# Optimization experiments

Measured on AMD Instinct MI355X. Metric: run time of the kernel, lower is better.

## Reference

```python
import jax, jax.numpy as jnp
import numpy as np

B, S, D, H = 4, 1024, 1024, 16
HS = D // H  # head_size = 64


def setup_inputs() -> dict:
    key = jax.random.key(0)
    ks = jax.random.split(key, 6)
    scale = 1.0 / np.sqrt(D)
    data = jax.random.normal(ks[0], (B, S, D), dtype=jnp.float32)
    # Per-head projection weights, stacked: [H, D, HS] (no bias, per nn.Linear(bias=False))
    Wq = jax.random.normal(ks[1], (H, D, HS), dtype=jnp.float32) * scale
    Wk = jax.random.normal(ks[2], (H, D, HS), dtype=jnp.float32) * scale
    Wv = jax.random.normal(ks[3], (H, D, HS), dtype=jnp.float32) * scale
    # Output projection: [H*HS, D] plus bias [D]
    Wo = jax.random.normal(ks[4], (H * HS, D), dtype=jnp.float32) * scale
    bo = jax.random.normal(ks[5], (D,), dtype=jnp.float32) * 0.01
    return {"data": data, "Wq": Wq, "Wk": Wk, "Wv": Wv, "Wo": Wo, "bo": bo}


def reference(data, Wq, Wk, Wv, Wo, bo):
    b, s, d = data.shape
    # Per-head Q/K/V projections (self-attention: encoder_data = data)
    q = jnp.einsum('bsd,hde->bhse', data, Wq)  # [B,H,S,HS]
    k = jnp.einsum('bsd,hde->bhse', data, Wk)
    v = jnp.einsum('bsd,hde->bhse', data, Wv)
    # NOTE: original scales by sqrt(embedding_dimension), not sqrt(head_size)
    scores = jnp.einsum('bhse,bhte->bhst', q, k) / jnp.sqrt(jnp.asarray(d, dtype=data.dtype))
    # causal mask (tril of block_size, sliced to [S, S])
    causal = jnp.tril(jnp.ones((s, s), dtype=bool))
    scores = jnp.where(causal, scores, -jnp.inf)
    attn = jax.nn.softmax(scores, axis=-1)  # dropout rate 0.0 -> identity
    out = jnp.einsum('bhst,bhte->bhse', attn, v)  # [B,H,S,HS]
    # concat heads along feature dim (head order matches ModuleList order)
    out = out.transpose(0, 2, 1, 3).reshape(b, s, -1)  # [B,S,H*HS]
    return out @ Wo + bo
```

## Files before the change

### kernel.cpp

```cpp
#include <hip/hip_runtime.h>
#include <hip/hip_bf16.h>
#include <stdint.h>

#define NEG_SENTINEL (-1e30f)

typedef short s16x8 __attribute__((ext_vector_type(8)));
typedef float f32x4 __attribute__((ext_vector_type(4)));

__device__ __forceinline__ ushort f2bf(float f) {
  union { float f; uint32_t u; } v; v.f = f;
  uint32_t u = v.u;
  u += 0x7fffu + ((u >> 16) & 1u);
  return (ushort)(u >> 16);
}
__device__ __forceinline__ ushort f2bf_rn(float f) {
  union { float f; uint32_t u; } v; v.f = f;
  return (ushort)((v.u + 0x8000u) >> 16);
}

__device__ __forceinline__ void async_ld16(ushort* lds, const ushort* g) {
  __builtin_amdgcn_global_load_lds(
      (const __attribute__((address_space(1))) uint32_t*)g,
      (__attribute__((address_space(3))) uint32_t*)lds, 16, 0, 0);
}

__global__ __launch_bounds__(256) void convert_f32_bf16(
    const float* __restrict__ src, ushort* __restrict__ dst) {
  long i = ((long)blockIdx.x * 256 + threadIdx.x) * 8;
  float4 a = *(const float4*)(src + i);
  float4 b = *(const float4*)(src + i + 4);
  union { ushort u[8]; uint4 v; } o;
  o.u[0] = f2bf(a.x); o.u[1] = f2bf(a.y); o.u[2] = f2bf(a.z); o.u[3] = f2bf(a.w);
  o.u[4] = f2bf(b.x); o.u[5] = f2bf(b.y); o.u[6] = f2bf(b.z); o.u[7] = f2bf(b.w);
  *(uint4*)(dst + i) = o.v;
}

__global__ __launch_bounds__(256) void transpose_w3(
    const float* __restrict__ Wq, const float* __restrict__ Wk,
    const float* __restrict__ Wv, ushort* __restrict__ WTall) {
  const int z = blockIdx.z;
  const int matsel = z >> 4;
  const float* src = (matsel == 0 ? Wq : (matsel == 1 ? Wk : Wv)) +
                     (long)(z & 15) * 65536;
  ushort* dst = WTall + (long)z * 65536;
  const int it = blockIdx.y;
  __shared__ __align__(16) ushort tile[64 * 72];
  const int tid = threadIdx.x;
#pragma unroll
  for (int p = 0; p < 4; ++p) {
    int chunk = tid + p * 256;
    int r = chunk >> 4, c0 = (chunk & 15) * 4;
    float4 f = *(const float4*)(src + (long)(it * 64 + r) * 64 + c0);
    union { ushort u[4]; uint2 v; } o;
    o.u[0] = f2bf(f.x); o.u[1] = f2bf(f.y); o.u[2] = f2bf(f.z); o.u[3] = f2bf(f.w);
    *(uint2*)&tile[r * 72 + c0] = o.v;
  }
  __syncthreads();
#pragma unroll
  for (int p = 0; p < 2; ++p) {
    int chunk = tid + p * 256;
    int r = chunk >> 3, c0 = (chunk & 7) * 8;
    union { ushort u[8]; uint4 v; } tmp;
#pragma unroll
    for (int k2 = 0; k2 < 8; ++k2) tmp.u[k2] = tile[(c0 + k2) * 72 + r];
    *(uint4*)(dst + (long)r * 1024 + it * 64 + c0) = tmp.v;
  }
}

__global__ __launch_bounds__(256) void transpose_cvt(
    const float* __restrict__ src, ushort* __restrict__ dst) {
  const int jt = blockIdx.x;
  const int it = blockIdx.y;
  __shared__ __align__(16) ushort tile[64 * 72];
  const int tid = threadIdx.x;
#pragma unroll
  for (int p = 0; p < 4; ++p) {
    int chunk = tid + p * 256;
    int r = chunk >> 4, c0 = (chunk & 15) * 4;
    float4 f = *(const float4*)(src + (long)(it * 64 + r) * 1024 + jt * 64 + c0);
    union { ushort u[4]; uint2 v; } o;
    o.u[0] = f2bf(f.x); o.u[1] = f2bf(f.y); o.u[2] = f2bf(f.z); o.u[3] = f2bf(f.w);
    *(uint2*)&tile[r * 72 + c0] = o.v;
  }
  __syncthreads();
#pragma unroll
  for (int p = 0; p < 2; ++p) {
    int chunk = tid + p * 256;
    int r = chunk >> 3, c0 = (chunk & 7) * 8;
    union { ushort u[8]; uint4 v; } tmp;
#pragma unroll
    for (int k2 = 0; k2 < 8; ++k2) tmp.u[k2] = tile[(c0 + k2) * 72 + r];
    *(uint4*)(dst + (long)(jt * 64 + r) * 1024 + it * 64 + c0) = tmp.v;
  }
}

__device__ __forceinline__ void gemm_core_128x128(
    const ushort* __restrict__ A, const ushort* __restrict__ BT,
    ushort* As, ushort* Bs, f32x4 acc[4][4]) {
  const int tid = threadIdx.x;
  const int lane = tid & 63, w = tid >> 6, quad = lane >> 4, l15 = lane & 15;
  const int wm = w >> 1, wn = w & 1;
  for (int k0 = 0; k0 < 1024; k0 += 64) {
#pragma unroll
    for (int p = 0; p < 4; ++p) {
      int c = tid + p * 256;
      int r = c >> 3, c8 = (c & 7) * 8;
      async_ld16(As + c * 8, A + (long)r * 1024 + k0 + c8);
      async_ld16(Bs + c * 8, BT + (long)r * 1024 + k0 + c8);
    }
    __syncthreads();
#pragma unroll
    for (int kk = 0; kk < 64; kk += 32) {
      s16x8 af[4], bfr[4];
#pragma unroll
      for (int mi = 0; mi < 4; ++mi)
        af[mi] = *(const s16x8*)&As[(wm * 64 + mi * 16 + l15) * 64 + kk + quad * 8];
#pragma unroll
      for (int ni = 0; ni < 4; ++ni)
        bfr[ni] = *(const s16x8*)&Bs[(wn * 64 + ni * 16 + l15) * 64 + kk + quad * 8];
#pragma unroll
      for (int mi = 0; mi < 4; ++mi)
#pragma unroll
        for (int ni = 0; ni < 4; ++ni)
          acc[mi][ni] = __builtin_amdgcn_mfma_f32_16x16x32_bf16(
              af[mi], bfr[ni], acc[mi][ni], 0, 0, 0);
    }
    __syncthreads();
  }
}

__global__ __launch_bounds__(256) void qkv_proj(
    const ushort* __restrict__ dataB, const ushort* __restrict__ WTall,
    ushort* __restrict__ QKV) {
  __shared__ __align__(16) ushort smem[128 * 136];
  ushort* As = smem;
  ushort* Bs = smem + 8192;
  ushort* Ct = smem;
  const int m0 = blockIdx.x * 128;
  const int n0 = blockIdx.y * 128;
  f32x4 acc[4][4];
  const f32x4 z = {0.f, 0.f, 0.f, 0.f};
#pragma unroll
  for (int mi = 0; mi < 4; ++mi)
#pragma unroll
    for (int ni = 0; ni < 4; ++ni) acc[mi][ni] = z;
  gemm_core_128x128(dataB + (long)m0 * 1024, WTall + (long)n0 * 1024, As, Bs, acc);

  const int tid = threadIdx.x;
  const int lane = tid & 63, w = tid >> 6, quad = lane >> 4, l15 = lane & 15;
  const int wm = w >> 1, wn = w & 1;
  const int matsel = n0 >> 10;
  const int bI = m0 >> 10, s0 = m0 & 1023;

  if (matsel < 2) {
    const float sc = (matsel == 0) ? 0.03125f : 1.0f;
    ushort* base = QKV + (long)matsel * 4194304 + (long)bI * 1048576;
#pragma unroll
    for (int mi = 0; mi < 4; ++mi) {
#pragma unroll
      for (int ni = 0; ni < 4; ++ni) {
        int n = n0 + wn * 64 + ni * 16 + l15;
        int h = (n >> 6) & 15, e = n & 63;
        ushort* col = base + (long)h * 65536 + e;
#pragma unroll
        for (int i = 0; i < 4; ++i) {
          int s = s0 + wm * 64 + mi * 16 + quad * 4 + i;
          col[s * 64] = f2bf(acc[mi][ni][i] * sc);
        }
      }
    }
  } else {
#pragma unroll
    for (int mi = 0; mi < 4; ++mi)
#pragma unroll
      for (int ni = 0; ni < 4; ++ni)
#pragma unroll
        for (int i = 0; i < 4; ++i)
          Ct[(wn * 64 + ni * 16 + l15) * 136 + wm * 64 + mi * 16 + quad * 4 + i] =
              f2bf(acc[mi][ni][i]);
    __syncthreads();
    ushort* base = QKV + 8388608 + (long)bI * 1048576;
#pragma unroll
    for (int p = 0; p < 8; ++p) {
      int c = tid + p * 256;
      int r = c >> 4, m8 = (c & 15) * 8;
      int h = ((n0 + r) >> 6) & 15, e = (n0 + r) & 63;
      *(uint4*)(base + (long)h * 65536 + e * 1024 + s0 + m8) =
          *(const uint4*)&Ct[r * 136 + m8];
    }
  }
}

__global__ __launch_bounds__(256) void out_proj(
    const ushort* __restrict__ Ocat, const ushort* __restrict__ WoT,
    const float* __restrict__ bo, float* __restrict__ out) {
  __shared__ __align__(16) ushort As[128 * 64];
  __shared__ __align__(16) ushort Bs[128 * 64];
  const int m0 = blockIdx.x * 128;
  const int n0 = blockIdx.y * 128;
  f32x4 acc[4][4];
  const f32x4 z = {0.f, 0.f, 0.f, 0.f};
#pragma unroll
  for (int mi = 0; mi < 4; ++mi)
#pragma unroll
    for (int ni = 0; ni < 4; ++ni) acc[mi][ni] = z;
  gemm_core_128x128(Ocat + (long)m0 * 1024, WoT + (long)n0 * 1024, As, Bs, acc);

  const int tid = threadIdx.x;
  const int lane = tid & 63, w = tid >> 6, quad = lane >> 4, l15 = lane & 15;
  const int wm = w >> 1, wn = w & 1;
#pragma unroll
  for (int mi = 0; mi < 4; ++mi) {
#pragma unroll
    for (int ni = 0; ni < 4; ++ni) {
#pragma unroll
      for (int i = 0; i < 4; ++i) {
        int m = m0 + wm * 64 + mi * 16 + quad * 4 + i;
        int n = n0 + wn * 64 + ni * 16 + l15;
        out[(long)m * 1024 + n] = acc[mi][ni][i] + bo[n];
      }
    }
  }
}

__global__ __launch_bounds__(512, 4) void attn_kernel(
    const ushort* __restrict__ QKV, ushort* __restrict__ Ocat) {
  __shared__ __align__(16) ushort Ks[128 * 72];
  __shared__ __align__(16) ushort Vs[64 * 136];
  __shared__ __align__(16) ushort Ps[8 * 16 * 136];
  const int qt = 7 - blockIdx.y;
  const int bh = blockIdx.x;
  const int b = bh >> 4, h = bh & 15;
  const int tid = threadIdx.x;
  const int w = tid >> 6, lane = tid & 63, quad = lane >> 4, l15 = lane & 15;
  const int q0 = qt * 128;

  const ushort* Qp = QKV + (long)bh * 65536;
  const ushort* Kp = QKV + 4194304 + (long)bh * 65536;
  const ushort* VTp = QKV + 8388608 + (long)bh * 65536;

  const int qrow = q0 + w * 16 + l15;
  s16x8 qf0 = *(const s16x8*)(Qp + (long)qrow * 64 + quad * 8);
  s16x8 qf1 = *(const s16x8*)(Qp + (long)qrow * 64 + 32 + quad * 8);

  f32x4 oacc[4];
  const f32x4 z = {0.f, 0.f, 0.f, 0.f};
#pragma unroll
  for (int et = 0; et < 4; ++et) oacc[et] = z;
  float l_i[4] = {0.f, 0.f, 0.f, 0.f};

  ushort* Psw = Ps + w * (16 * 136);
  const int nj = qt + 1;

  for (int j = 0; j < nj; ++j) {
#pragma unroll
    for (int p = 0; p < 2; ++p) {
      int c = tid + p * 512;
      { int r = c >> 3, c8 = (c & 7) * 8;
        *(uint4*)&Ks[r * 72 + c8] = *(const uint4*)(Kp + (long)(j * 128 + r) * 64 + c8); }
      { int r = c >> 4, c8 = (c & 15) * 8;
        *(uint4*)&Vs[r * 136 + c8] = *(const uint4*)(VTp + (long)r * 1024 + j * 128 + c8); }
    }
    __syncthreads();

    f32x4 sacc[8];
#pragma unroll
    for (int nt = 0; nt < 8; ++nt) sacc[nt] = z;
#pragma unroll
    for (int kk = 0; kk < 64; kk += 32) {
      s16x8 a = kk ? qf1 : qf0;
#pragma unroll
      for (int nt = 0; nt < 8; ++nt) {
        s16x8 bfr = *(const s16x8*)&Ks[(nt * 16 + l15) * 72 + kk + quad * 8];
        sacc[nt] = __builtin_amdgcn_mfma_f32_16x16x32_bf16(a, bfr, sacc[nt], 0, 0, 0);
      }
    }

    if (j == qt) {
      const int srow = q0 + w * 16 + quad * 4;
#pragma unroll
      for (int nt = 0; nt < 8; ++nt) {
#pragma unroll
        for (int i = 0; i < 4; ++i) {
          int tg = j * 128 + nt * 16 + l15;
          if (tg > srow + i) sacc[nt][i] = NEG_SENTINEL;
        }
      }
    }

#pragma unroll
    for (int i = 0; i < 4; ++i) {
#pragma unroll
      for (int nt = 0; nt < 8; ++nt) {
        float p = __expf(sacc[nt][i]);
        Psw[(quad * 4 + i) * 136 + nt * 16 + l15] = f2bf_rn(p);
        l_i[i] += p;
      }
    }

#pragma unroll
    for (int kk = 0; kk < 128; kk += 32) {
      s16x8 pa = *(const s16x8*)&Psw[l15 * 136 + kk + quad * 8];
#pragma unroll
      for (int et = 0; et < 4; ++et) {
        s16x8 vb = *(const s16x8*)&Vs[(et * 16 + l15) * 136 + kk + quad * 8];
        oacc[et] = __builtin_amdgcn_mfma_f32_16x16x32_bf16(pa, vb, oacc[et], 0, 0, 0);
      }
    }
    __syncthreads();
  }

#pragma unroll
  for (int i = 0; i < 4; ++i) {
#pragma unroll
    for (int d = 1; d < 16; d <<= 1) l_i[i] += __shfl_xor(l_i[i], d, 64);
  }

  ushort* Ob = Ocat + ((long)(b * 1024 + q0 + w * 16) * 1024) + h * 64;
#pragma unroll
  for (int et = 0; et < 4; ++et) {
#pragma unroll
    for (int i = 0; i < 4; ++i) {
      float denom = l_i[i];
      float v = oacc[et][i] / (denom > 0.f ? denom : 1.0f);
      Ob[(long)(quad * 4 + i) * 1024 + et * 16 + l15] = f2bf_rn(v);
    }
  }
}

extern "C" void kernel_launch(void* const* d_in, const int* in_sizes, int n_in,
                              void* d_out, int out_size, void* d_ws, size_t ws_size,
                              hipStream_t stream) {
  const float* data = (const float*)d_in[0];
  const float* Wq = (const float*)d_in[1];
  const float* Wk = (const float*)d_in[2];
  const float* Wv = (const float*)d_in[3];
  const float* Wo = (const float*)d_in[4];
  const float* bo = (const float*)d_in[5];
  float* out = (float*)d_out;

  ushort* ws = (ushort*)d_ws;
  ushort* QKV = ws;
  ushort* dataB = ws + 12582912;
  ushort* Ocat = ws + 16777216;
  ushort* WTall = ws + 20971520;
  ushort* WoT = ws + 20971520 + 3145728;

  dim3 blk(256);
  convert_f32_bf16<<<dim3(2048), blk, 0, stream>>>(data, dataB);
  transpose_w3<<<dim3(1, 16, 48), blk, 0, stream>>>(Wq, Wk, Wv, WTall);
  transpose_cvt<<<dim3(16, 16), blk, 0, stream>>>(Wo, WoT);
  qkv_proj<<<dim3(32, 24), blk, 0, stream>>>(dataB, WTall, QKV);
  attn_kernel<<<dim3(64, 8), dim3(512), 0, stream>>>(QKV, Ocat);
  out_proj<<<dim3(32, 8), blk, 0, stream>>>(Ocat, WoT, bo, out);
}
```

Measured before the change: 186.8 us.

## Rewrite QKV projection as 256x256-tile GEMM with async double-buffered LDS pipeline

Replaces the 128x128 QKV projection kernel with a 512-thread 256x256-tile GEMM. It uses swizzled LDS, global_load_lds double buffering with the next K-slab prefetched while MFMAs run, explicit barrier/waitcnt scheduling and setprio around the MFMA clusters. The V-transpose epilogue now writes 8-byte stores directly instead of going through an LDS staging buffer. This is meant to raise MFMA utilisation and data reuse in the largest GEMM. In exchange it adds much more register pressure (a 32-accumulator tile), 128KB of LDS per block, and a grid of only 192 blocks, which risks low occupancy and load imbalance across the CUs.

After: 175.7 us. 5.9% less time.

```diff
diff --git a/kernel.cpp b/kernel.cpp
--- a/kernel.cpp
+++ b/kernel.cpp
@@ -129,64 +129,161 @@
   }
 }
 
-__global__ __launch_bounds__(256) void qkv_proj(
+#define BAR() do { asm volatile("" ::: "memory"); \
+  __builtin_amdgcn_s_barrier(); \
+  asm volatile("" ::: "memory"); } while (0)
+#define LGKM0() do { asm volatile("s_waitcnt lgkmcnt(0)" ::: "memory"); \
+  __builtin_amdgcn_sched_barrier(0); } while (0)
+#define STAGE2(LDSB, G) do { \
+  async_ld16((LDSB) + o0, (G) + so0); \
+  async_ld16((LDSB) + o0 + 4096, (G) + so0 + 65536); } while (0)
+#define LD_A(PA, MIB) do { \
+  _Pragma("unroll") for (int dm = 0; dm < 4; ++dm) { \
+    afr[dm][0] = *(const s16x8*)((PA) + ((MIB) + dm) * 1024); \
+    afr[dm][1] = *(const s16x8*)((PA) + ((MIB) + dm) * 1024 + 512); } } while (0)
+#define LD_B(PB, NIB) do { \
+  _Pragma("unroll") for (int dn = 0; dn < 2; ++dn) { \
+    bfr[(NIB) + dn][0] = *(const s16x8*)((PB) + ((NIB) + dn) * 1024); \
+    bfr[(NIB) + dn][1] = *(const s16x8*)((PB) + ((NIB) + dn) * 1024 + 512); } } while (0)
+#define MFMA_Q(MIB, NIB) do { \
+  __builtin_amdgcn_s_setprio(1); \
+  _Pragma("unroll") for (int kg = 0; kg < 2; ++kg) \
+    _Pragma("unroll") for (int dm = 0; dm < 4; ++dm) \
+      _Pragma("unroll") for (int dn = 0; dn < 2; ++dn) \
+        acc[(MIB) + dm][(NIB) + dn] = __builtin_amdgcn_mfma_f32_16x16x32_bf16( \
+            afr[dm][kg], bfr[(NIB) + dn][kg], acc[(MIB) + dm][(NIB) + dn], 0, 0, 0); \
+  __builtin_amdgcn_s_setprio(0); } while (0)
+
+__global__ __launch_bounds__(512, 2) void qkv_proj256(
     const ushort* __restrict__ dataB, const ushort* __restrict__ WTall,
     ushort* __restrict__ QKV) {
-  __shared__ __align__(16) ushort smem[128 * 136];
-  ushort* As = smem;
-  ushort* Bs = smem + 8192;
-  ushort* Ct = smem;
-  const int m0 = blockIdx.x * 128;
-  const int n0 = blockIdx.y * 128;
-  f32x4 acc[4][4];
+  __shared__ __align__(16) ushort smem[65536];
+  const int tid = threadIdx.x;
+  const int lane = tid & 63, w = tid >> 6, quad = lane >> 4, l15 = lane & 15;
+  const int wm = w >> 2, wn = w & 3;
+  const int m0 = blockIdx.x * 256;
+  const int n0 = blockIdx.y * 256;
+
+  const int o0 = tid * 8;
+  {
+  }
+  const int st_ = o0 >> 9, u_ = o0 & 511;
+  const int u0_ = u_ ^ (((u_ >> 8) & 1) << 4);
+  const long so0 = (long)((st_ >> 1) * 16 + (u0_ >> 5)) * 1024 +
+                   (st_ & 1) * 32 + (u0_ & 31);
+
+  const ushort* Ab = dataB + (long)m0 * 1024;
+  const ushort* Bb = WTall + (long)n0 * 1024;
+
+  const int alane = (l15 * 32 + quad * 8) ^ (((l15 >> 3) & 1) << 4);
+  const ushort* pA0 = smem + wm * 8192 + alane;
+  const ushort* pB0 = smem + 16384 + (wn >> 1) * 8192 + (wn & 1) * 4096 + alane;
+  const ushort* pA1 = pA0 + 32768;
+  const ushort* pB1 = pB0 + 32768;
+
+  f32x4 acc[8][4];
   const f32x4 z = {0.f, 0.f, 0.f, 0.f};
 #pragma unroll
-  for (int mi = 0; mi < 4; ++mi)
+  for (int mi = 0; mi < 8; ++mi)
 #pragma unroll
     for (int ni = 0; ni < 4; ++ni) acc[mi][ni] = z;
-  gemm_core_128x128(dataB + (long)m0 * 1024, WTall + (long)n0 * 1024, As, Bs, acc);
-
-  const int tid = threadIdx.x;
-  const int lane = tid & 63, w = tid >> 6, quad = lane >> 4, l15 = lane & 15;
-  const int wm = w >> 1, wn = w & 1;
+
+  s16x8 afr[4][2];
+  s16x8 bfr[4][2];
+
+  STAGE2(smem + 16384, Bb);
+  STAGE2(smem + 16384 + 8192, Bb + 131072);
+  STAGE2(smem, Ab);
+  STAGE2(smem + 8192, Ab + 131072);
+  STAGE2(smem + 32768 + 16384, Bb + 64);
+  STAGE2(smem + 32768 + 16384 + 8192, Bb + 131072 + 64);
+  asm volatile("s_waitcnt vmcnt(4)" ::: "memory");
+  BAR();
+
+#pragma unroll 1
+  for (int it = 0; it < 8; ++it) {
+    const int t0k = it * 128;
+    const bool sN = (it < 7);
+    LD_A(pA0, 0); LD_B(pB0, 0);
+    STAGE2(smem + 32768, Ab + t0k + 64);
+    asm volatile("s_waitcnt lgkmcnt(8)" ::: "memory");
+    BAR(); LGKM0();
+    MFMA_Q(0, 0);
+    BAR();
+    LD_B(pB0, 2);
+    STAGE2(smem + 32768 + 8192, Ab + 131072 + t0k + 64);
+    BAR(); LGKM0();
+    MFMA_Q(0, 2);
+    BAR();
+    LD_A(pA0, 4);
+    if (sN) STAGE2(smem + 16384, Bb + t0k + 128);
+    BAR(); LGKM0();
+    MFMA_Q(4, 0);
+    BAR();
+    if (sN) STAGE2(smem + 16384 + 8192, Bb + 131072 + t0k + 128);
+    BAR(); LGKM0();
+    MFMA_Q(4, 2);
+    if (sN) { asm volatile("s_waitcnt vmcnt(4)" ::: "memory"); }
+    else    { asm volatile("s_waitcnt vmcnt(0)" ::: "memory"); }
+    BAR();
+    LD_A(pA1, 0); LD_B(pB1, 0);
+    if (sN) STAGE2(smem, Ab + t0k + 128);
+    asm volatile("s_waitcnt lgkmcnt(8)" ::: "memory");
+    BAR(); LGKM0();
+    MFMA_Q(0, 0);
+    BAR();
+    LD_B(pB1, 2);
+    if (sN) STAGE2(smem + 8192, Ab + 131072 + t0k + 128);
+    BAR(); LGKM0();
+    MFMA_Q(0, 2);
+    BAR();
+    LD_A(pA1, 4);
+    if (sN) STAGE2(smem + 32768 + 16384, Bb + t0k + 192);
+    BAR(); LGKM0();
+    MFMA_Q(4, 0);
+    BAR();
+    if (sN) STAGE2(smem + 32768 + 16384 + 8192, Bb + 131072 + t0k + 192);
+    BAR(); LGKM0();
+    MFMA_Q(4, 2);
+    if (sN) {
+      asm volatile("s_waitcnt vmcnt(4)" ::: "memory");
+      BAR();
+    }
+  }
+
   const int matsel = n0 >> 10;
   const int bI = m0 >> 10, s0 = m0 & 1023;
-
+  const int nloc0 = (n0 & 1023) + wn * 64;
   if (matsel < 2) {
     const float sc = (matsel == 0) ? 0.03125f : 1.0f;
     ushort* base = QKV + (long)matsel * 4194304 + (long)bI * 1048576;
 #pragma unroll
-    for (int mi = 0; mi < 4; ++mi) {
+    for (int mi = 0; mi < 8; ++mi) {
 #pragma unroll
       for (int ni = 0; ni < 4; ++ni) {
-        int n = n0 + wn * 64 + ni * 16 + l15;
-        int h = (n >> 6) & 15, e = n & 63;
+        int n = nloc0 + ni * 16 + l15;
+        int h = n >> 6, e = n & 63;
         ushort* col = base + (long)h * 65536 + e;
-#pragma unroll
-        for (int i = 0; i < 4; ++i) {
-          int s = s0 + wm * 64 + mi * 16 + quad * 4 + i;
-          col[s * 64] = f2bf(acc[mi][ni][i] * sc);
-        }
+        int sb = s0 + wm * 128 + mi * 16 + quad * 4;
+#pragma unroll
+        for (int i = 0; i < 4; ++i)
+          col[(long)(sb + i) * 64] = f2bf(acc[mi][ni][i] * sc);
       }
     }
   } else {
-#pragma unroll
-    for (int mi = 0; mi < 4; ++mi)
-#pragma unroll
-      for (int ni = 0; ni < 4; ++ni)
-#pragma unroll
-        for (int i = 0; i < 4; ++i)
-          Ct[(wn * 64 + ni * 16 + l15) * 136 + wm * 64 + mi * 16 + quad * 4 + i] =
-              f2bf(acc[mi][ni][i]);
-    __syncthreads();
     ushort* base = QKV + 8388608 + (long)bI * 1048576;
 #pragma unroll
-    for (int p = 0; p < 8; ++p) {
-      int c = tid + p * 256;
-      int r = c >> 4, m8 = (c & 15) * 8;
-      int h = ((n0 + r) >> 6) & 15, e = (n0 + r) & 63;
-      *(uint4*)(base + (long)h * 65536 + e * 1024 + s0 + m8) =
-          *(const uint4*)&Ct[r * 136 + m8];
+    for (int mi = 0; mi < 8; ++mi) {
+#pragma unroll
+      for (int ni = 0; ni < 4; ++ni) {
+        int n = nloc0 + ni * 16 + l15;
+        int h = n >> 6, e = n & 63;
+        int sb = s0 + wm * 128 + mi * 16 + quad * 4;
+        union { ushort u[4]; uint2 v; } o;
+#pragma unroll
+        for (int i = 0; i < 4; ++i) o.u[i] = f2bf(acc[mi][ni][i]);
+        *(uint2*)(base + (long)h * 65536 + (long)e * 1024 + sb) = o.v;
+      }
     }
   }
 }
@@ -350,7 +447,7 @@
   convert_f32_bf16<<<dim3(2048), blk, 0, stream>>>(data, dataB);
   transpose_w3<<<dim3(1, 16, 48), blk, 0, stream>>>(Wq, Wk, Wv, WTall);
   transpose_cvt<<<dim3(16, 16), blk, 0, stream>>>(Wo, WoT);
-  qkv_proj<<<dim3(32, 24), blk, 0, stream>>>(dataB, WTall, QKV);
+  qkv_proj256<<<dim3(16, 12), dim3(512), 0, stream>>>(dataB, WTall, QKV);
   attn_kernel<<<dim3(64, 8), dim3(512), 0, stream>>>(QKV, Ocat);
   out_proj<<<dim3(32, 8), blk, 0, stream>>>(Ocat, WoT, bo, out);
 }
```
